# Kernel optimization log

Measured on AMD Instinct MI355X. Metric: run time of the kernel, lower is better.

## Reference

```python
import jax, jax.numpy as jnp
import numpy as np

ROIALIGN = (7, 7)   # args.roialign_size
SCALE = 0.125       # args.spatial_scale
SR = 2              # roi_align sampling ratio (fixed; torchvision uses adaptive when -1)


def _conv2d(x, w, b, pad):
    y = jax.lax.conv_general_dilated(x, w, (1, 1), pad,
                                     dimension_numbers=('NCHW', 'OIHW', 'NCHW'))
    return y + b[None, :, None, None]


def _bilinear(f, ys, xs):
    # f: [C,H,W]; ys: [Ny]; xs: [Nx] -> [C,Ny,Nx]
    C, H, W = f.shape
    y = jnp.clip(ys, 0.0, H - 1.0)
    x = jnp.clip(xs, 0.0, W - 1.0)
    y0 = jnp.floor(y).astype(jnp.int32)
    x0 = jnp.floor(x).astype(jnp.int32)
    y1 = jnp.minimum(y0 + 1, H - 1)
    x1 = jnp.minimum(x0 + 1, W - 1)
    wy = (y - y0)[None, :, None]
    wx = (x - x0)[None, None, :]
    f00 = f[:, y0[:, None], x0[None, :]]
    f01 = f[:, y0[:, None], x1[None, :]]
    f10 = f[:, y1[:, None], x0[None, :]]
    f11 = f[:, y1[:, None], x1[None, :]]
    return f00 * (1 - wy) * (1 - wx) + f01 * (1 - wy) * wx + f10 * wy * (1 - wx) + f11 * wy * wx


def _roi_align(feat, rois):
    # feat: [N,C,H,W]; rois: [K,5] = (batch_idx, x1, y1, x2, y2) in image coords
    rh, rw = ROIALIGN
    C = feat.shape[1]

    def one(box, bidx):
        f = feat[bidx]
        x1, y1, x2, y2 = box * SCALE
        bh = (y2 - y1) / rh
        bw = (x2 - x1) / rw
        ys = y1 + (jnp.arange(rh * SR, dtype=feat.dtype) + 0.5) / SR * bh
        xs = x1 + (jnp.arange(rw * SR, dtype=feat.dtype) + 0.5) / SR * bw
        s = _bilinear(f, ys, xs)                       # [C, rh*SR, rw*SR]
        return s.reshape(C, rh, SR, rw, SR).mean(axis=(2, 4))

    return jax.vmap(one)(rois[:, 1:5], rois[:, 0].astype(jnp.int32))


def setup_inputs() -> dict:
    key = jax.random.key(0)
    ks = jax.random.split(key, 16)
    N, M, H, W = 4, 48, 96, 96
    cor_planes = 4 * (2 * 4 + 1) ** 2  # 324
    corr = jax.random.normal(ks[0], (N, cor_planes, H, W), jnp.float32)

    def make_det(k):
        k1, k2, k3, k4, k5, k6 = jax.random.split(k, 6)
        cx = jax.random.uniform(k1, (N, M), minval=80.0, maxval=688.0)
        cy = jax.random.uniform(k2, (N, M), minval=80.0, maxval=688.0)
        w = jax.random.uniform(k3, (N, M), minval=24.0, maxval=120.0)
        h = jax.random.uniform(k4, (N, M), minval=24.0, maxval=120.0)
        valid = jnp.where(jax.random.uniform(k5, (N, M)) < 0.9, 1.0, -1.0)
        ids = jax.random.randint(k6, (N, M), 0, 100).astype(jnp.float32)
        pad = jnp.zeros((N, M, 4), jnp.float32)
        cols = [valid, ids, cx, cy, w, h]
        return jnp.concatenate([c[..., None] for c in cols] + [pad], axis=-1)

    detection1 = make_det(ks[1])
    detection2 = make_det(ks[2])

    def p(k, shape):
        return (jax.random.normal(k, shape, jnp.float32) * 0.02)

    return {
        'corr': corr,
        'detection1_': detection1,
        'detection1': detection1,
        'detection2': detection2,
        'convc1_w': p(ks[3], (256, cor_planes, 1, 1)), 'convc1_b': jnp.zeros(256, jnp.float32),
        'convc2_w': p(ks[4], (256, 256, 3, 3)), 'convc2_b': jnp.zeros(256, jnp.float32),
        'conv_w': p(ks[5], (128, 256, 3, 3)), 'conv_b': jnp.zeros(128, jnp.float32),
        'head_conv_w': p(ks[6], (256, 132, 7, 7)), 'head_conv_b': jnp.zeros(256, jnp.float32),
        'fc6_w': p(ks[7], (256, 256)), 'fc6_b': jnp.zeros(256, jnp.float32),
        'fc7_w': p(ks[8], (256, 256)), 'fc7_b': jnp.zeros(256, jnp.float32),
        'cls_w': p(ks[9], (1, 256)), 'cls_b': jnp.zeros(1, jnp.float32),
    }


def reference(corr, detection1_, detection1, detection2,
              convc1_w, convc1_b, convc2_w, convc2_b, conv_w, conv_b,
              head_conv_w, head_conv_b, fc6_w, fc6_b, fc7_w, fc7_b, cls_w, cls_b):
    N, M = detection1.shape[0], detection1.shape[1]
    rh, rw = ROIALIGN
    # CompressConv
    c = jax.nn.relu(_conv2d(corr, convc1_w, convc1_b, 'VALID'))
    c = jax.nn.relu(_conv2d(c, convc2_w, convc2_b, [(1, 1), (1, 1)]))
    rel = jax.nn.relu(_conv2d(c, conv_w, conv_b, [(1, 1), (1, 1)]))   # [N,128,H,W]

    def to_xyxy(d):
        xy1 = d[..., 2:4] - d[..., 4:6] / 2
        xy2 = xy1 + d[..., 4:6]
        return jnp.concatenate([d[..., :2], xy1, xy2, d[..., 6:]], axis=-1)

    d1 = to_xyxy(detection1)
    d2 = to_xyxy(detection2)
    bidx = jnp.broadcast_to(jnp.arange(N, dtype=d1.dtype)[:, None], (N, M))
    rois = jnp.concatenate([bidx[..., None], d1[..., 2:6]], axis=-1).reshape(N * M, 5)
    rf = _roi_align(rel, rois)                                        # [N*M,128,7,7]

    d_ = jnp.concatenate([
        jnp.broadcast_to(d1[..., :8][:, :, None, :], (N, M, M, 8)),
        jnp.broadcast_to(d2[..., :8][:, None, :, :], (N, M, M, 8)),
    ], axis=-1).reshape(N * M * M, 16)

    # position encoding: 4 relative-geometry channels tiled over the ROI grid
    eps = 1e-6
    cx1 = (d_[:, 2] + d_[:, 4]) * 0.5; cy1 = (d_[:, 3] + d_[:, 5]) * 0.5
    w1 = jnp.maximum(d_[:, 4] - d_[:, 2], eps); h1 = jnp.maximum(d_[:, 5] - d_[:, 3], eps)
    cx2 = (d_[:, 10] + d_[:, 12]) * 0.5; cy2 = (d_[:, 11] + d_[:, 13]) * 0.5
    w2 = jnp.maximum(d_[:, 12] - d_[:, 10], eps); h2 = jnp.maximum(d_[:, 13] - d_[:, 11], eps)
    pos4 = jnp.stack([(cx2 - cx1) / w1, (cy2 - cy1) / h1,
                      jnp.log(w2 / w1), jnp.log(h2 / h1)], axis=-1)   # [NMM,4]
    pos = jnp.broadcast_to(pos4[:, :, None, None], (N * M * M, 4, rh, rw))

    rf_exp = jnp.broadcast_to(rf[:, None], (N * M, M, 128, rh, rw)).reshape(N * M * M, 128, rh, rw)
    data = jnp.concatenate([rf_exp, pos], axis=1)                     # [NMM,132,7,7]

    labels = (d_[:, 1] == d_[:, 9]).astype(jnp.float32)
    valid = (d_[:, 0] != -1) & (d_[:, 8] != -1)

    # ConvMLPHead (scores for invalid pairs are simply masked out by `valid`)
    x = _conv2d(data, head_conv_w, head_conv_b, 'VALID').reshape(N * M * M, -1)
    x = jax.nn.relu(x @ fc6_w.T + fc6_b)
    x = jax.nn.relu(x @ fc7_w.T + fc7_b)
    scores = x @ cls_w.T + cls_b                                      # [NMM,1]
    return scores, labels, valid
```

## Files before the change

kernel.cpp:

```cpp
#include <hip/hip_runtime.h>
#include <hip/hip_bf16.h>

#define NB    4
#define HH    96
#define WW    96
#define PIX   9216
#define C0    324
#define MM    48
#define NROI  192
#define NPAIR 9216
#define KHEAD 6468
#define KRF   6272
#define SPLITS 28
#define CPS    7

#define CWSTG 18432

typedef unsigned short u16;
typedef __attribute__((ext_vector_type(8))) short bf16x8;
typedef __attribute__((ext_vector_type(4))) float f32x4;
typedef __attribute__((ext_vector_type(16))) float f32x16;
typedef __attribute__((ext_vector_type(4))) unsigned short u16x4;
typedef __attribute__((ext_vector_type(4))) int i32x4;

__device__ __forceinline__ u16 f2bf(float f) {
    __hip_bfloat16 h = __float2bfloat16(f);
    union { __hip_bfloat16 h; u16 u; } c; c.h = h; return c.u;
}
__device__ __forceinline__ float b2f(u16 u) {
    union { unsigned int i; float f; } c; c.i = ((unsigned int)u) << 16; return c.f;
}

__global__ __launch_bounds__(256) void zero_halo(u16* __restrict__ a1, u16* __restrict__ a2)
{
    int idx = blockIdx.x * 256 + threadIdx.x;
    int c8 = idx & 31;
    int t = idx >> 5;
    int h = t % 388, img = t / 388;
    u16* base = (img & 4) ? a2 : a1;
    int b = img & 3;
    int y, x;
    if (h < 98)       { y = 0;  x = h; }
    else if (h < 196) { y = 97; x = h - 98; }
    else { int r = (h - 196) >> 1; x = ((h - 196) & 1) * 97; y = 1 + r; }
    long long off = (((long long)(b * 98 + y)) * 98 + x) * 256 + c8 * 8;
    i32x4 z = {0, 0, 0, 0};
    *(i32x4*)(base + off) = z;
}

__global__ __launch_bounds__(256) void prep_all(
    const float* __restrict__ c1w, const float* __restrict__ c2w,
    const float* __restrict__ c3w, const float* __restrict__ hw,
    const float* __restrict__ f6w, const float* __restrict__ f7w,
    u16* __restrict__ wt1f, u16* __restrict__ wt2f, u16* __restrict__ wt3f,
    u16* __restrict__ wtHt, u16* __restrict__ w6c, u16* __restrict__ w7c,
    float* __restrict__ wsum4)
{
    int blk = blockIdx.x, tid = threadIdx.x;
    if (blk < 352) {
        int idx = blk * 256 + tid;
        if (idx >= 90112) return;
        int j = idx & 7, lane = (idx >> 3) & 63, ot = (idx >> 9) & 7, ks = idx >> 12;
        int oc = ot * 32 + (lane & 31);
        int k = ks * 16 + (lane >> 5) * 8 + j;
        wt1f[idx] = f2bf((k < C0) ? c1w[oc * C0 + k] : 0.f);
    } else if (blk < 2656) {
        int idx = (blk - 352) * 256 + tid;
        int j = idx & 7, lane = (idx >> 3) & 63, ot = (idx >> 9) & 3;
        int t = idx >> 11;
        int tap = t % 9; t /= 9;
        int icb = t & 15, ocb = t >> 4;
        int oc = ocb * 128 + ot * 32 + (lane & 31);
        int ic = icb * 16 + (lane >> 5) * 8 + j;
        wt2f[idx] = f2bf(c2w[(oc * 256 + ic) * 9 + tap]);
    } else if (blk < 3808) {
        int idx = (blk - 2656) * 256 + tid;
        int j = idx & 7, lane = (idx >> 3) & 63, ot = (idx >> 9) & 3;
        int t = idx >> 11;
        int tap = t % 9; int icb = t / 9;
        int oc = ot * 32 + (lane & 31);
        int ic = icb * 16 + (lane >> 5) * 8 + j;
        wt3f[idx] = f2bf(c3w[(oc * 256 + ic) * 9 + tap]);
    } else if (blk < 10080) {
        int idx = (blk - 3808) * 256 + tid;
        int oc = idx / KRF, r = idx % KRF;
        int s = r >> 7, c = r & 127;
        wtHt[idx] = f2bf(hw[oc * KHEAD + c * 49 + s]);
    } else if (blk < 10336) {
        int idx = (blk - 10080) * 256 + tid;
        w6c[idx] = f2bf(f6w[idx]);
    } else if (blk < 10592) {
        int idx = (blk - 10336) * 256 + tid;
        w7c[idx] = f2bf(f7w[idx]);
    } else {
        int idx = (blk - 10592) * 256 + tid;
        if (idx >= 1024) return;
        int oc = idx >> 2, j = idx & 3;
        const float* p = hw + (long long)oc * KHEAD + (128 + j) * 49;
        float s = 0.f;
        #pragma unroll
        for (int t = 0; t < 49; ++t) s += p[t];
        wsum4[idx] = s;
    }
}

__global__ __launch_bounds__(256) void conv1_v2(
    const float* __restrict__ corr, const u16* __restrict__ wf,
    const float* __restrict__ bias, u16* __restrict__ outp)
{
    __shared__ __align__(16) u16 Ws1[8192];
    __shared__ __align__(16) u16 Bs[64 * 40];
    const int tid = threadIdx.x;
    const int b = blockIdx.y;
    const int p0 = blockIdx.x * 64;
    const int lane = tid & 63, wid = tid >> 6;
    const int n = lane & 31, half = lane >> 5;
    const int wocw = wid & 1, wpx = wid >> 1;
    const int kr = tid >> 3, pxg = tid & 7;

    f32x16 acc[4];
    #pragma unroll
    for (int i = 0; i < 4; ++i)
        #pragma unroll
        for (int e = 0; e < 16; ++e) acc[i][e] = 0.f;

    float4 s0 = {0,0,0,0}, s1 = {0,0,0,0};
    if (kr < C0) {
        const float* src = &corr[((long long)(b * C0 + kr)) * PIX + p0 + pxg * 8];
        s0 = *(const float4*)src; s1 = *(const float4*)(src + 4);
    }
    bf16x8 wr[4];
    #pragma unroll
    for (int i = 0; i < 4; ++i) wr[i] = *(const bf16x8*)(wf + (i * 256 + tid) * 8);

    for (int kc = 0; kc < 11; ++kc) {
        __syncthreads();
        Bs[(pxg * 8 + 0) * 40 + kr] = f2bf(s0.x);
        Bs[(pxg * 8 + 1) * 40 + kr] = f2bf(s0.y);
        Bs[(pxg * 8 + 2) * 40 + kr] = f2bf(s0.z);
        Bs[(pxg * 8 + 3) * 40 + kr] = f2bf(s0.w);
        Bs[(pxg * 8 + 4) * 40 + kr] = f2bf(s1.x);
        Bs[(pxg * 8 + 5) * 40 + kr] = f2bf(s1.y);
        Bs[(pxg * 8 + 6) * 40 + kr] = f2bf(s1.z);
        Bs[(pxg * 8 + 7) * 40 + kr] = f2bf(s1.w);
        #pragma unroll
        for (int i = 0; i < 4; ++i) *(bf16x8*)&Ws1[(i * 256 + tid) * 8] = wr[i];
        __syncthreads();
        if (kc < 10) {
            int k = (kc + 1) * 32 + kr;
            if (k < C0) {
                const float* src = &corr[((long long)(b * C0 + k)) * PIX + p0 + pxg * 8];
                s0 = *(const float4*)src; s1 = *(const float4*)(src + 4);
            } else { s0 = (float4){0,0,0,0}; s1 = (float4){0,0,0,0}; }
            const u16* wn = wf + (kc + 1) * 8192;
            #pragma unroll
            for (int i = 0; i < 4; ++i) wr[i] = *(const bf16x8*)(wn + (i * 256 + tid) * 8);
        }
        #pragma unroll
        for (int ks = 0; ks < 2; ++ks) {
            bf16x8 bb = *(const bf16x8*)&Bs[(wpx * 32 + n) * 40 + ks * 16 + half * 8];
            #pragma unroll
            for (int ot = 0; ot < 4; ++ot) {
                bf16x8 a = *(const bf16x8*)&Ws1[((ks * 8 + wocw * 4 + ot) * 64 + lane) * 8];
                acc[ot] = __builtin_amdgcn_mfma_f32_32x32x16_bf16(a, bb, acc[ot], 0, 0, 0);
            }
        }
    }
    const int px = p0 + wpx * 32 + n;
    const int y = px / 96, x = px % 96;
    const long long obase = (((long long)(b * 98 + y + 1)) * 98 + x + 1) * 256;
    #pragma unroll
    for (int ot = 0; ot < 4; ++ot) {
        int ocb = wocw * 128 + ot * 32;
        f32x16 d = acc[ot];
        #pragma unroll
        for (int r2 = 0; r2 < 4; ++r2) {
            int oc4 = ocb + r2 * 8 + half * 4;
            f32x4 bv = *(const f32x4*)(bias + oc4);
            u16x4 pk;
            #pragma unroll
            for (int g = 0; g < 4; ++g) pk[g] = f2bf(fmaxf(d[r2 * 4 + g] + bv[g], 0.f));
            *(u16x4*)(outp + obase + oc4) = pk;
        }
    }
}

template<int COUT, bool PADOUT>
__global__ __launch_bounds__(256, 2) void conv3x3_v2(
    const u16* __restrict__ inp, const u16* __restrict__ wf,
    const float* __restrict__ bias, u16* __restrict__ outp)
{
    __shared__ __align__(16) u16 Ws[CWSTG];
    __shared__ __align__(16) u16 Hs[204 * 24];
    const int tid = threadIdx.x;
    const int b = blockIdx.z;
    const int x0 = (blockIdx.x % 3) * 32, y0 = (blockIdx.x / 3) * 4;
    const int lane = tid & 63, wid = tid >> 6;
    const int n = lane & 31, half = lane >> 5;
    const int woc = wid & 1, wpx = wid >> 1;

    const u16* wsrc = wf + (size_t)blockIdx.y * 16 * CWSTG;
    const bool hstager = tid < 204;
    const int hrow = tid / 34, hcol = tid % 34;
    const u16* hsrc = inp + (((size_t)(b * 98 + y0 + hrow)) * 98 + x0 + hcol) * 256;

    f32x16 acc[2][2];
    #pragma unroll
    for (int i = 0; i < 2; ++i)
        #pragma unroll
        for (int r = 0; r < 2; ++r)
            #pragma unroll
            for (int e = 0; e < 16; ++e) acc[i][r][e] = 0.f;

    bf16x8 wreg[9];
    bf16x8 h0, h1;
    #pragma unroll
    for (int it = 0; it < 9; ++it)
        wreg[it] = *(const bf16x8*)(wsrc + (it * 256 + tid) * 8);
    if (hstager) { h0 = *(const bf16x8*)hsrc; h1 = *(const bf16x8*)(hsrc + 8); }

    for (int icb = 0; icb < 16; ++icb) {
        __syncthreads();
        #pragma unroll
        for (int it = 0; it < 9; ++it)
            *(bf16x8*)&Ws[(it * 256 + tid) * 8] = wreg[it];
        if (hstager) {
            *(bf16x8*)&Hs[tid * 24]     = h0;
            *(bf16x8*)&Hs[tid * 24 + 8] = h1;
        }
        __syncthreads();
        if (icb < 15) {
            const u16* wn = wsrc + (size_t)(icb + 1) * CWSTG;
            #pragma unroll
            for (int it = 0; it < 9; ++it)
                wreg[it] = *(const bf16x8*)(wn + (it * 256 + tid) * 8);
            if (hstager) {
                const u16* hn = hsrc + (icb + 1) * 16;
                h0 = *(const bf16x8*)hn; h1 = *(const bf16x8*)(hn + 8);
            }
        }
        bf16x8 bfr[4][3];
        #pragma unroll
        for (int rr = 0; rr < 4; ++rr)
            #pragma unroll
            for (int dx = 0; dx < 3; ++dx)
                bfr[rr][dx] = *(const bf16x8*)&Hs[((wpx * 2 + rr) * 34 + dx + n) * 24 + half * 8];
        #pragma unroll
        for (int tap = 0; tap < 9; ++tap) {
            const int dy = tap / 3, dx = tap % 3;
            bf16x8 a0 = *(const bf16x8*)&Ws[((tap * 4 + woc * 2 + 0) * 64 + lane) * 8];
            bf16x8 a1 = *(const bf16x8*)&Ws[((tap * 4 + woc * 2 + 1) * 64 + lane) * 8];
            #pragma unroll
            for (int r = 0; r < 2; ++r) {
                acc[0][r] = __builtin_amdgcn_mfma_f32_32x32x16_bf16(a0, bfr[r + dy][dx], acc[0][r], 0, 0, 0);
                acc[1][r] = __builtin_amdgcn_mfma_f32_32x32x16_bf16(a1, bfr[r + dy][dx], acc[1][r], 0, 0, 0);
            }
        }
    }
    #pragma unroll
    for (int ot = 0; ot < 2; ++ot) {
        int ocb = blockIdx.y * 128 + woc * 64 + ot * 32;
        #pragma unroll
        for (int r = 0; r < 2; ++r) {
            int y = y0 + wpx * 2 + r;
            int x = x0 + n;
            f32x16 d = acc[ot][r];
            long long obase;
            if (PADOUT) obase = (((long long)(b * 98 + y + 1)) * 98 + x + 1) * COUT;
            else        obase = (((long long)(b * 96 + y)) * 96 + x) * COUT;
            #pragma unroll
            for (int r2 = 0; r2 < 4; ++r2) {
                int oc4 = ocb + r2 * 8 + half * 4;
                f32x4 bv = *(const f32x4*)(bias + oc4);
                u16x4 pk;
                #pragma unroll
                for (int g = 0; g < 4; ++g) pk[g] = f2bf(fmaxf(d[r2 * 4 + g] + bv[g], 0.f));
                *(u16x4*)(outp + obase + oc4) = pk;
            }
        }
    }
}

__global__ __launch_bounds__(256) void roi_align_cl(
    const u16* __restrict__ rel, const float* __restrict__ det1,
    u16* __restrict__ rf)
{
    const int roi = blockIdx.x, tid = threadIdx.x;
    const int c = tid & 127, sb = tid >> 7;
    const int b = roi / MM, m = roi % MM;
    const float* d = det1 + (long long)(b * MM + m) * 10;
    float cx = d[2], cy = d[3], w = d[4], h = d[5];
    float x1f = cx - w * 0.5f, y1f = cy - h * 0.5f;
    float x1 = x1f * 0.125f, y1 = y1f * 0.125f;
    float x2 = (x1f + w) * 0.125f, y2 = (y1f + h) * 0.125f;
    float bh = (y2 - y1) * (1.f / 7.f), bw = (x2 - x1) * (1.f / 7.f);
    const u16* fb = rel + (long long)b * PIX * 128 + c;
    for (int s = sb; s < 49; s += 2) {
        int i = s / 7, j = s % 7;
        float sum = 0.f;
        #pragma unroll
        for (int di = 0; di < 2; ++di) {
            float y = y1 + ((float)(2 * i + di) + 0.5f) * 0.5f * bh;
            y = fminf(fmaxf(y, 0.f), 95.f);
            int yy0 = (int)floorf(y);
            int yy1 = min(yy0 + 1, 95);
            float wy = y - (float)yy0;
            #pragma unroll
            for (int dj = 0; dj < 2; ++dj) {
                float x = x1 + ((float)(2 * j + dj) + 0.5f) * 0.5f * bw;
                x = fminf(fmaxf(x, 0.f), 95.f);
                int xx0 = (int)floorf(x);
                int xx1 = min(xx0 + 1, 95);
                float wx = x - (float)xx0;
                float f00 = b2f(fb[((long long)yy0 * 96 + xx0) * 128]);
                float f01 = b2f(fb[((long long)yy0 * 96 + xx1) * 128]);
                float f10 = b2f(fb[((long long)yy1 * 96 + xx0) * 128]);
                float f11 = b2f(fb[((long long)yy1 * 96 + xx1) * 128]);
                sum += f00 * (1.f - wy) * (1.f - wx) + f01 * (1.f - wy) * wx
                     + f10 * wy * (1.f - wx) + f11 * wy * wx;
            }
        }
        rf[(long long)roi * KRF + s * 128 + c] = f2bf(sum * 0.25f);
    }
}

__global__ __launch_bounds__(256) void head_gemm_mfma(
    const u16* __restrict__ rf, const u16* __restrict__ wtHt,
    float* __restrict__ Gpart)
{
    __shared__ __align__(16) u16 As[64 * 40];
    __shared__ __align__(16) u16 Bs[128 * 40];
    const int tid = threadIdx.x;
    const int rb = blockIdx.x >> 1, ob = blockIdx.x & 1;
    const int split = blockIdx.y;
    const int lane = tid & 63, wid = tid >> 6;
    const int q = lane >> 4, m16 = lane & 15;
    const int wr = wid & 1, wo = wid >> 1;

    const int arl = tid >> 2, aqd = tid & 3;
    const u16* abase = rf + (long long)(rb * 64 + arl) * KRF + aqd * 8;
    const int bol0 = tid >> 2, bqd = tid & 3;
    const u16* bbase0 = wtHt + (long long)(ob * 128 + bol0) * KRF + bqd * 8;
    const u16* bbase1 = bbase0 + 64LL * KRF;

    f32x4 acc[2][4];
    #pragma unroll
    for (int i = 0; i < 2; ++i)
        #pragma unroll
        for (int j = 0; j < 4; ++j) acc[i][j] = (f32x4){0.f, 0.f, 0.f, 0.f};

    int k0 = split * CPS * 32;
    bf16x8 ra = *(const bf16x8*)(abase + k0);
    bf16x8 rb0 = *(const bf16x8*)(bbase0 + k0);
    bf16x8 rb1 = *(const bf16x8*)(bbase1 + k0);
    for (int cch = 0; cch < CPS; ++cch) {
        __syncthreads();
        *(bf16x8*)&As[arl * 40 + aqd * 8] = ra;
        *(bf16x8*)&Bs[bol0 * 40 + bqd * 8] = rb0;
        *(bf16x8*)&Bs[(64 + bol0) * 40 + bqd * 8] = rb1;
        __syncthreads();
        if (cch < CPS - 1) {
            int kn = k0 + (cch + 1) * 32;
            ra  = *(const bf16x8*)(abase + kn);
            rb0 = *(const bf16x8*)(bbase0 + kn);
            rb1 = *(const bf16x8*)(bbase1 + kn);
        }
        bf16x8 a[2], bb[4];
        #pragma unroll
        for (int rt = 0; rt < 2; ++rt)
            a[rt] = *(const bf16x8*)&As[(wr * 32 + rt * 16 + m16) * 40 + q * 8];
        #pragma unroll
        for (int ot = 0; ot < 4; ++ot)
            bb[ot] = *(const bf16x8*)&Bs[(wo * 64 + ot * 16 + m16) * 40 + q * 8];
        #pragma unroll
        for (int rt = 0; rt < 2; ++rt)
            #pragma unroll
            for (int ot = 0; ot < 4; ++ot)
                acc[rt][ot] = __builtin_amdgcn_mfma_f32_16x16x32_bf16(a[rt], bb[ot], acc[rt][ot], 0, 0, 0);
    }
    #pragma unroll
    for (int rt = 0; rt < 2; ++rt)
        #pragma unroll
        for (int ot = 0; ot < 4; ++ot) {
            int oc = ob * 128 + wo * 64 + ot * 16 + m16;
            #pragma unroll
            for (int rg = 0; rg < 4; ++rg) {
                int roi = rb * 64 + wr * 32 + rt * 16 + q * 4 + rg;
                Gpart[((long long)split * NROI + roi) * 256 + oc] = acc[rt][ot][rg];
            }
        }
}

__global__ __launch_bounds__(256) void reduce_G_kernel(
    const float* __restrict__ Gpart, float* __restrict__ G)
{
    int idx = blockIdx.x * 256 + threadIdx.x;
    float s = 0.f;
    #pragma unroll
    for (int sp = 0; sp < SPLITS; ++sp) s += Gpart[(long long)sp * NROI * 256 + idx];
    G[idx] = s;
}

#define PHS 272
__global__ __launch_bounds__(256) void pair_head(
    const float* __restrict__ G, const float* __restrict__ d1,
    const float* __restrict__ d2, const float* __restrict__ wsum4,
    const float* __restrict__ hb,
    const u16* __restrict__ w6, const float* __restrict__ b6,
    const u16* __restrict__ w7, const float* __restrict__ b7,
    const float* __restrict__ cw, const float* __restrict__ cb,
    float* __restrict__ scores, float* __restrict__ labels,
    float* __restrict__ valid)
{
    __shared__ __align__(16) u16 bufA[64 * PHS];
    __shared__ __align__(16) u16 bufB[64 * PHS];
    __shared__ float Gs[2][256];
    __shared__ float ps[64][4];
    __shared__ float clw[256];

    const int tid = threadIdx.x;
    const int p0 = blockIdx.x * 64;
    const int r0 = p0 / MM;
    const int lane = tid & 63, w = tid >> 6;
    const int q = lane >> 4, m16 = lane & 15;

    clw[tid] = cw[tid];
    #pragma unroll
    for (int l = 0; l < 2; ++l) {
        int idx = tid + l * 256;
        int rr = idx >> 8, col = idx & 255;
        Gs[rr][col] = G[min(r0 + rr, NROI - 1) * 256 + col];
    }
    if (tid < 64) {
        int pair = p0 + tid;
        int b = pair / (MM * MM); int rem = pair % (MM * MM);
        int m1 = rem / MM, m2 = rem % MM;
        const float* rA = d1 + (long long)(b * MM + m1) * 10;
        const float* rB = d2 + (long long)(b * MM + m2) * 10;
        float v1 = rA[0], id1 = rA[1], cxa = rA[2], cya = rA[3], wa = rA[4], ha = rA[5];
        float v2 = rB[0], id2 = rB[1], cxb = rB[2], cyb = rB[3], wb = rB[4], hbv = rB[5];
        const float eps = 1e-6f;
        float ax1 = cxa - wa * 0.5f, ay1 = cya - ha * 0.5f;
        float ax2 = ax1 + wa,        ay2 = ay1 + ha;
        float bx1 = cxb - wb * 0.5f, by1 = cyb - hbv * 0.5f;
        float bx2 = bx1 + wb,        by2 = by1 + hbv;
        float ccx1 = (ax1 + ax2) * 0.5f, ccy1 = (ay1 + ay2) * 0.5f;
        float ww1 = fmaxf(ax2 - ax1, eps), hh1 = fmaxf(ay2 - ay1, eps);
        float ccx2 = (bx1 + bx2) * 0.5f, ccy2 = (by1 + by2) * 0.5f;
        float ww2 = fmaxf(bx2 - bx1, eps), hh2 = fmaxf(by2 - by1, eps);
        ps[tid][0] = (ccx2 - ccx1) / ww1;
        ps[tid][1] = (ccy2 - ccy1) / hh1;
        ps[tid][2] = logf(ww2 / ww1);
        ps[tid][3] = logf(hh2 / hh1);
        labels[pair] = (id1 == id2) ? 1.f : 0.f;
        valid[pair]  = (v1 != -1.f && v2 != -1.f) ? 1.f : 0.f;
    }
    __syncthreads();

    #pragma unroll
    for (int it = 0; it < 16; ++it) {
        int idx = tid + it * 256;
        int px = idx >> 6, o4 = (idx & 63) * 4;
        int rl = (p0 + px) / MM - r0;
        f32x4 g = *(const f32x4*)&Gs[rl][o4];
        f32x4 hv = *(const f32x4*)&hb[o4];
        f32x4 p4 = *(const f32x4*)&ps[px][0];
        u16x4 pk;
        #pragma unroll
        for (int j = 0; j < 4; ++j) {
            f32x4 w4 = *(const f32x4*)&wsum4[(o4 + j) * 4];
            float v = g[j] + hv[j] + p4[0] * w4[0] + p4[1] * w4[1] + p4[2] * w4[2] + p4[3] * w4[3];
            pk[j] = f2bf(v);
        }
        *(u16x4*)&bufA[px * PHS + o4] = pk;
    }
    __syncthreads();

    #pragma unroll
    for (int layer = 0; layer < 2; ++layer) {
        const u16* wgt = layer ? w7 : w6;
        const float* bs = layer ? b7 : b6;
        const u16* src = layer ? bufB : bufA;
        u16* dst = layer ? bufA : bufB;
        f32x4 acc[4][4];
        #pragma unroll
        for (int i = 0; i < 4; ++i)
            #pragma unroll
            for (int j = 0; j < 4; ++j) acc[i][j] = (f32x4){0.f, 0.f, 0.f, 0.f};
        #pragma unroll
        for (int kc = 0; kc < 8; ++kc) {
            bf16x8 a[4], bb[4];
            #pragma unroll
            for (int i = 0; i < 4; ++i)
                a[i] = *(const bf16x8*)&wgt[(w * 64 + i * 16 + m16) * 256 + kc * 32 + q * 8];
            #pragma unroll
            for (int pt = 0; pt < 4; ++pt)
                bb[pt] = *(const bf16x8*)&src[(pt * 16 + m16) * PHS + kc * 32 + q * 8];
            #pragma unroll
            for (int i = 0; i < 4; ++i)
                #pragma unroll
                for (int pt = 0; pt < 4; ++pt)
                    acc[i][pt] = __builtin_amdgcn_mfma_f32_16x16x32_bf16(a[i], bb[pt], acc[i][pt], 0, 0, 0);
        }
        #pragma unroll
        for (int i = 0; i < 4; ++i) {
            int oc4 = w * 64 + i * 16 + q * 4;
            f32x4 bv = *(const f32x4*)(bs + oc4);
            #pragma unroll
            for (int pt = 0; pt < 4; ++pt) {
                int px = pt * 16 + m16;
                f32x4 dd = acc[i][pt];
                u16x4 pk;
                #pragma unroll
                for (int rg = 0; rg < 4; ++rg)
                    pk[rg] = f2bf(fmaxf(dd[rg] + bv[rg], 0.f));
                *(u16x4*)&dst[px * PHS + oc4] = pk;
            }
        }
        __syncthreads();
    }

    {
        int px = tid >> 2, qq = tid & 3;
        float acc = 0.f;
        #pragma unroll
        for (int k8 = 0; k8 < 8; ++k8) {
            bf16x8 hv = *(const bf16x8*)&bufA[px * PHS + qq * 64 + k8 * 8];
            #pragma unroll
            for (int e = 0; e < 8; ++e)
                acc += b2f((u16)hv[e]) * clw[qq * 64 + k8 * 8 + e];
        }
        acc += __shfl_xor(acc, 1, 64);
        acc += __shfl_xor(acc, 2, 64);
        if (qq == 0) scores[p0 + px] = acc + cb[0];
    }
}

extern "C" void kernel_launch(void* const* d_in, const int* in_sizes, int n_in,
                              void* d_out, int out_size, void* d_ws, size_t ws_size,
                              hipStream_t stream) {
    const float* corr   = (const float*)d_in[0];
    const float* det1   = (const float*)d_in[2];
    const float* det2   = (const float*)d_in[3];
    const float* c1w    = (const float*)d_in[4];
    const float* c1b    = (const float*)d_in[5];
    const float* c2w    = (const float*)d_in[6];
    const float* c2b    = (const float*)d_in[7];
    const float* c3w    = (const float*)d_in[8];
    const float* c3b    = (const float*)d_in[9];
    const float* hw     = (const float*)d_in[10];
    const float* hbias  = (const float*)d_in[11];
    const float* f6w    = (const float*)d_in[12];
    const float* f6b    = (const float*)d_in[13];
    const float* f7w    = (const float*)d_in[14];
    const float* f7b    = (const float*)d_in[15];
    const float* clsw   = (const float*)d_in[16];
    const float* clsb   = (const float*)d_in[17];
    float* out = (float*)d_out;

    char* base = (char*)d_ws;
    auto alloc = [&](size_t bytes) { char* p = base; base += (bytes + 255) & ~(size_t)255; return p; };

    const size_t ACTP_BYTES = (size_t)NB * 98 * 98 * 256 * 2;
    u16*   act1p = (u16*)  alloc(ACTP_BYTES);
    u16*   act2p = (u16*)  alloc(ACTP_BYTES);
    u16*   rel   = (u16*)  alloc((size_t)NB * PIX * 128 * 2);
    u16*   wt1f  = (u16*)  alloc((size_t)90112 * 2);
    u16*   wt2f  = (u16*)  alloc((size_t)2 * 16 * CWSTG * 2);
    u16*   wt3f  = (u16*)  alloc((size_t)16 * CWSTG * 2);
    u16*   wtHt  = (u16*)  alloc((size_t)256 * KRF * 2);
    u16*   w6c   = (u16*)  alloc(256 * 256 * 2);
    u16*   w7c   = (u16*)  alloc(256 * 256 * 2);
    float* wsum4 = (float*)alloc(256 * 4 * 4);
    u16*   rf    = (u16*)  alloc((size_t)NROI * KRF * 2);
    float* Gpart = (float*)alloc((size_t)SPLITS * NROI * 256 * 4);
    float* G     = (float*)alloc(NROI * 256 * 4);

    float* scores_out = out;
    float* labels_out = out + NPAIR;
    float* valid_out  = out + 2 * NPAIR;

    zero_halo<<<388, 256, 0, stream>>>(act1p, act2p);
    prep_all<<<10596, 256, 0, stream>>>(c1w, c2w, c3w, hw, f6w, f7w,
                                        wt1f, wt2f, wt3f, wtHt, w6c, w7c, wsum4);
    conv1_v2<<<dim3(144, NB), 256, 0, stream>>>(corr, wt1f, c1b, act1p);
    conv3x3_v2<256, true><<<dim3(72, 2, NB), 256, 0, stream>>>(act1p, wt2f, c2b, act2p);
    conv3x3_v2<128, false><<<dim3(72, 1, NB), 256, 0, stream>>>(act2p, wt3f, c3b, rel);
    roi_align_cl<<<NROI, 256, 0, stream>>>(rel, det1, rf);
    head_gemm_mfma<<<dim3(6, SPLITS), 256, 0, stream>>>(rf, wtHt, Gpart);
    reduce_G_kernel<<<NROI, 256, 0, stream>>>(Gpart, G);
    pair_head<<<144, 256, 0, stream>>>(G, det1, det2, wsum4, hbias,
                                       w6c, f6b, w7c, f7b, clsw, clsb,
                                       scores_out, labels_out, valid_out);
}
```

Measured before the change: 289.3 us.

## Merge halo zeroing into LDS-staged weight prep, fuse G reduction into pair head

The weight-prep kernel is rewritten so each block loads contiguous float4 rows into shared memory and writes transposed bf16 fragments as 8-wide vectors. This replaces the scattered per-element gathers and cuts the grid from about 10.6k blocks to 732, and it also absorbs the halo-zeroing kernel. The split-K reduction of G is folded into pair_head, which removes a launch and an intermediate buffer, but each pair_head block now reads all 28 partial sums for its ROIs redundantly. The conv3x3 kernel preloads all 18 A fragments from LDS before the MFMA loop, which adds register pressure under launch_bounds(256,2).

```diff
diff --git a/kernel.cpp b/kernel.cpp
--- a/kernel.cpp
+++ b/kernel.cpp
@@ -21,6 +21,7 @@
 typedef __attribute__((ext_vector_type(4))) float f32x4;
 typedef __attribute__((ext_vector_type(16))) float f32x16;
 typedef __attribute__((ext_vector_type(4))) unsigned short u16x4;
+typedef __attribute__((ext_vector_type(8))) unsigned short u16x8;
 typedef __attribute__((ext_vector_type(4))) int i32x4;
 
 __device__ __forceinline__ u16 f2bf(float f) {
@@ -31,76 +32,143 @@
     union { unsigned int i; float f; } c; c.i = ((unsigned int)u) << 16; return c.f;
 }
 
-__global__ __launch_bounds__(256) void zero_halo(u16* __restrict__ a1, u16* __restrict__ a2)
-{
-    int idx = blockIdx.x * 256 + threadIdx.x;
-    int c8 = idx & 31;
-    int t = idx >> 5;
-    int h = t % 388, img = t / 388;
-    u16* base = (img & 4) ? a2 : a1;
-    int b = img & 3;
-    int y, x;
-    if (h < 98)       { y = 0;  x = h; }
-    else if (h < 196) { y = 97; x = h - 98; }
-    else { int r = (h - 196) >> 1; x = ((h - 196) & 1) * 97; y = 1 + r; }
-    long long off = (((long long)(b * 98 + y)) * 98 + x) * 256 + c8 * 8;
-    i32x4 z = {0, 0, 0, 0};
-    *(i32x4*)(base + off) = z;
-}
-
-__global__ __launch_bounds__(256) void prep_all(
+__global__ __launch_bounds__(256) void prep_v2(
     const float* __restrict__ c1w, const float* __restrict__ c2w,
     const float* __restrict__ c3w, const float* __restrict__ hw,
     const float* __restrict__ f6w, const float* __restrict__ f7w,
     u16* __restrict__ wt1f, u16* __restrict__ wt2f, u16* __restrict__ wt3f,
     u16* __restrict__ wtHt, u16* __restrict__ w6c, u16* __restrict__ w7c,
-    float* __restrict__ wsum4)
+    float* __restrict__ wsum4, u16* __restrict__ a1, u16* __restrict__ a2)
 {
-    int blk = blockIdx.x, tid = threadIdx.x;
-    if (blk < 352) {
-        int idx = blk * 256 + tid;
-        if (idx >= 90112) return;
-        int j = idx & 7, lane = (idx >> 3) & 63, ot = (idx >> 9) & 7, ks = idx >> 12;
-        int oc = ot * 32 + (lane & 31);
-        int k = ks * 16 + (lane >> 5) * 8 + j;
-        wt1f[idx] = f2bf((k < C0) ? c1w[oc * C0 + k] : 0.f);
-    } else if (blk < 2656) {
-        int idx = (blk - 352) * 256 + tid;
-        int j = idx & 7, lane = (idx >> 3) & 63, ot = (idx >> 9) & 3;
-        int t = idx >> 11;
-        int tap = t % 9; t /= 9;
-        int icb = t & 15, ocb = t >> 4;
-        int oc = ocb * 128 + ot * 32 + (lane & 31);
-        int ic = icb * 16 + (lane >> 5) * 8 + j;
-        wt2f[idx] = f2bf(c2w[(oc * 256 + ic) * 9 + tap]);
-    } else if (blk < 3808) {
-        int idx = (blk - 2656) * 256 + tid;
-        int j = idx & 7, lane = (idx >> 3) & 63, ot = (idx >> 9) & 3;
-        int t = idx >> 11;
-        int tap = t % 9; int icb = t / 9;
-        int oc = ot * 32 + (lane & 31);
-        int ic = icb * 16 + (lane >> 5) * 8 + j;
-        wt3f[idx] = f2bf(c3w[(oc * 256 + ic) * 9 + tap]);
-    } else if (blk < 10080) {
-        int idx = (blk - 3808) * 256 + tid;
-        int oc = idx / KRF, r = idx % KRF;
-        int s = r >> 7, c = r & 127;
-        wtHt[idx] = f2bf(hw[oc * KHEAD + c * 49 + s]);
-    } else if (blk < 10336) {
-        int idx = (blk - 10080) * 256 + tid;
-        w6c[idx] = f2bf(f6w[idx]);
-    } else if (blk < 10592) {
-        int idx = (blk - 10336) * 256 + tid;
-        w7c[idx] = f2bf(f7w[idx]);
+    __shared__ u16 L[18432];
+    const int blk = blockIdx.x, tid = threadIdx.x;
+
+    if (blk < 8) {
+        const int ot = blk;
+        const float* src = c1w + (size_t)ot * 32 * C0;
+        for (int it = 0; it < 11; ++it) {
+            int i = tid + it * 256;
+            if (i < 2592) {
+                float4 v = *(const float4*)(src + i * 4);
+                int n = i / 81, k4 = (i % 81) * 4;
+                L[n * 324 + k4 + 0] = f2bf(v.x);
+                L[n * 324 + k4 + 1] = f2bf(v.y);
+                L[n * 324 + k4 + 2] = f2bf(v.z);
+                L[n * 324 + k4 + 3] = f2bf(v.w);
+            }
+        }
+        __syncthreads();
+        for (int it = 0; it < 6; ++it) {
+            int v = tid + it * 256;
+            if (v >= 1408) break;
+            int ks = v >> 6, lane = v & 63;
+            int n = lane & 31, half = lane >> 5;
+            u16x8 pk;
+            #pragma unroll
+            for (int j = 0; j < 8; ++j) {
+                int k = ks * 16 + half * 8 + j;
+                pk[j] = (k < C0) ? L[n * 324 + k] : (u16)0;
+            }
+            *(u16x8*)&wt1f[((ks * 8 + ot) * 64 + lane) * 8] = pk;
+        }
+    } else if (blk < 56) {
+        const bool is2 = blk < 40;
+        const int b8 = is2 ? (blk - 8) : (blk - 40);
+        const int oc8 = b8 * 8;
+        const int ocb = oc8 >> 7;
+        const int ot = (oc8 >> 5) & 3;
+        const int nb = oc8 & 31;
+        const float* src = (is2 ? c2w : c3w) + (size_t)oc8 * 2304;
+        u16* dst = is2 ? wt2f : wt3f;
+        for (int it = 0; it < 18; ++it) {
+            int i = tid + it * 256;
+            float4 v = *(const float4*)(src + i * 4);
+            int n = i / 576, t4 = (i % 576) * 4;
+            L[n * 2304 + t4 + 0] = f2bf(v.x);
+            L[n * 2304 + t4 + 1] = f2bf(v.y);
+            L[n * 2304 + t4 + 2] = f2bf(v.z);
+            L[n * 2304 + t4 + 3] = f2bf(v.w);
+        }
+        __syncthreads();
+        for (int it = 0; it < 9; ++it) {
+            int v = tid + it * 256;
+            int o8 = v & 7; int rest = v >> 3;
+            int half = rest & 1; rest >>= 1;
+            int tap = rest % 9; int icb = rest / 9;
+            int lane = half * 32 + nb + o8;
+            u16x8 pk;
+            #pragma unroll
+            for (int j = 0; j < 8; ++j) {
+                int ic = icb * 16 + half * 8 + j;
+                pk[j] = L[o8 * 2304 + ic * 9 + tap];
+            }
+            size_t dest = ((((size_t)(ocb * 16 + icb) * 9 + tap) * 4 + ot) * 64 + lane) * 8;
+            *(u16x8*)&dst[dest] = pk;
+        }
+    } else if (blk < 312) {
+        const int oc = blk - 56;
+        const float* src = hw + (size_t)oc * KHEAD;
+        for (int it = 0; it < 7; ++it) {
+            int i = tid + it * 256;
+            if (i < 1617) {
+                float4 v = *(const float4*)(src + i * 4);
+                L[i * 4 + 0] = f2bf(v.x);
+                L[i * 4 + 1] = f2bf(v.y);
+                L[i * 4 + 2] = f2bf(v.z);
+                L[i * 4 + 3] = f2bf(v.w);
+            }
+        }
+        if (tid < 4) {
+            const float* p = src + (128 + tid) * 49;
+            float s = 0.f;
+            #pragma unroll
+            for (int t = 0; t < 49; ++t) s += p[t];
+            wsum4[oc * 4 + tid] = s;
+        }
+        __syncthreads();
+        for (int it = 0; it < 4; ++it) {
+            int v = tid + it * 256;
+            if (v >= 784) break;
+            u16x8 pk;
+            #pragma unroll
+            for (int j = 0; j < 8; ++j) {
+                int r = v * 8 + j;
+                int s = r >> 7, c = r & 127;
+                pk[j] = L[c * 49 + s];
+            }
+            *(u16x8*)&wtHt[(size_t)oc * KRF + v * 8] = pk;
+        }
+    } else if (blk < 344) {
+        const bool is6 = blk < 328;
+        const int b = is6 ? (blk - 312) : (blk - 328);
+        const float* src = (is6 ? f6w : f7w) + (size_t)(b * 256 + tid) * 16;
+        u16* dst = (is6 ? w6c : w7c) + (size_t)(b * 256 + tid) * 16;
+        u16x8 pk0, pk1;
+        #pragma unroll
+        for (int h = 0; h < 2; ++h) {
+            float4 v0 = *(const float4*)(src + h * 8);
+            float4 v1 = *(const float4*)(src + h * 8 + 4);
+            u16x8 pk;
+            pk[0] = f2bf(v0.x); pk[1] = f2bf(v0.y); pk[2] = f2bf(v0.z); pk[3] = f2bf(v0.w);
+            pk[4] = f2bf(v1.x); pk[5] = f2bf(v1.y); pk[6] = f2bf(v1.z); pk[7] = f2bf(v1.w);
+            if (h == 0) pk0 = pk; else pk1 = pk;
+        }
+        *(u16x8*)(dst + 0) = pk0;
+        *(u16x8*)(dst + 8) = pk1;
     } else {
-        int idx = (blk - 10592) * 256 + tid;
-        if (idx >= 1024) return;
-        int oc = idx >> 2, j = idx & 3;
-        const float* p = hw + (long long)oc * KHEAD + (128 + j) * 49;
-        float s = 0.f;
-        #pragma unroll
-        for (int t = 0; t < 49; ++t) s += p[t];
-        wsum4[idx] = s;
+        int idx = (blk - 344) * 256 + tid;
+        int c8 = idx & 31;
+        int t = idx >> 5;
+        int h = t % 388, img = t / 388;
+        u16* base = (img & 4) ? a2 : a1;
+        int b = img & 3;
+        int y, x;
+        if (h < 98)       { y = 0;  x = h; }
+        else if (h < 196) { y = 97; x = h - 98; }
+        else { int r = (h - 196) >> 1; x = ((h - 196) & 1) * 97; y = 1 + r; }
+        long long off = (((long long)(b * 98 + y)) * 98 + x) * 256 + c8 * 8;
+        i32x4 z = {0, 0, 0, 0};
+        *(i32x4*)(base + off) = z;
     }
 }
 
@@ -186,7 +254,7 @@
 }
 
 template<int COUT, bool PADOUT>
-__global__ __launch_bounds__(256, 2) void conv3x3_v2(
+__global__ __launch_bounds__(256, 2) void conv3x3_v3(
     const u16* __restrict__ inp, const u16* __restrict__ wf,
     const float* __restrict__ bias, u16* __restrict__ outp)
 {
@@ -239,6 +307,12 @@
                 h0 = *(const bf16x8*)hn; h1 = *(const bf16x8*)(hn + 8);
             }
         }
+        bf16x8 afr[9][2];
+        #pragma unroll
+        for (int tap = 0; tap < 9; ++tap)
+            #pragma unroll
+            for (int j = 0; j < 2; ++j)
+                afr[tap][j] = *(const bf16x8*)&Ws[((tap * 4 + woc * 2 + j) * 64 + lane) * 8];
         bf16x8 bfr[4][3];
         #pragma unroll
         for (int rr = 0; rr < 4; ++rr)
@@ -248,12 +322,10 @@
         #pragma unroll
         for (int tap = 0; tap < 9; ++tap) {
             const int dy = tap / 3, dx = tap % 3;
-            bf16x8 a0 = *(const bf16x8*)&Ws[((tap * 4 + woc * 2 + 0) * 64 + lane) * 8];
-            bf16x8 a1 = *(const bf16x8*)&Ws[((tap * 4 + woc * 2 + 1) * 64 + lane) * 8];
             #pragma unroll
             for (int r = 0; r < 2; ++r) {
-                acc[0][r] = __builtin_amdgcn_mfma_f32_32x32x16_bf16(a0, bfr[r + dy][dx], acc[0][r], 0, 0, 0);
-                acc[1][r] = __builtin_amdgcn_mfma_f32_32x32x16_bf16(a1, bfr[r + dy][dx], acc[1][r], 0, 0, 0);
+                acc[0][r] = __builtin_amdgcn_mfma_f32_32x32x16_bf16(afr[tap][0], bfr[r + dy][dx], acc[0][r], 0, 0, 0);
+                acc[1][r] = __builtin_amdgcn_mfma_f32_32x32x16_bf16(afr[tap][1], bfr[r + dy][dx], acc[1][r], 0, 0, 0);
             }
         }
     }
@@ -391,19 +463,9 @@
         }
 }
 
-__global__ __launch_bounds__(256) void reduce_G_kernel(
-    const float* __restrict__ Gpart, float* __restrict__ G)
-{
-    int idx = blockIdx.x * 256 + threadIdx.x;
-    float s = 0.f;
-    #pragma unroll
-    for (int sp = 0; sp < SPLITS; ++sp) s += Gpart[(long long)sp * NROI * 256 + idx];
-    G[idx] = s;
-}
-
 #define PHS 272
 __global__ __launch_bounds__(256) void pair_head(
-    const float* __restrict__ G, const float* __restrict__ d1,
+    const float* __restrict__ Gpart, const float* __restrict__ d1,
     const float* __restrict__ d2, const float* __restrict__ wsum4,
     const float* __restrict__ hb,
     const u16* __restrict__ w6, const float* __restrict__ b6,
@@ -429,7 +491,12 @@
     for (int l = 0; l < 2; ++l) {
         int idx = tid + l * 256;
         int rr = idx >> 8, col = idx & 255;
-        Gs[rr][col] = G[min(r0 + rr, NROI - 1) * 256 + col];
+        int roi = min(r0 + rr, NROI - 1);
+        float s = 0.f;
+        #pragma unroll
+        for (int sp = 0; sp < SPLITS; ++sp)
+            s += Gpart[((long long)sp * NROI + roi) * 256 + col];
+        Gs[rr][col] = s;
     }
     if (tid < 64) {
         int pair = p0 + tid;
@@ -574,22 +641,20 @@
     float* wsum4 = (float*)alloc(256 * 4 * 4);
     u16*   rf    = (u16*)  alloc((size_t)NROI * KRF * 2);
     float* Gpart = (float*)alloc((size_t)SPLITS * NROI * 256 * 4);
-    float* G     = (float*)alloc(NROI * 256 * 4);
 
     float* scores_out = out;
     float* labels_out = out + NPAIR;
     float* valid_out  = out + 2 * NPAIR;
 
-    zero_halo<<<388, 256, 0, stream>>>(act1p, act2p);
-    prep_all<<<10596, 256, 0, stream>>>(c1w, c2w, c3w, hw, f6w, f7w,
-                                        wt1f, wt2f, wt3f, wtHt, w6c, w7c, wsum4);
+    prep_v2<<<732, 256, 0, stream>>>(c1w, c2w, c3w, hw, f6w, f7w,
+                                     wt1f, wt2f, wt3f, wtHt, w6c, w7c, wsum4,
+                                     act1p, act2p);
     conv1_v2<<<dim3(144, NB), 256, 0, stream>>>(corr, wt1f, c1b, act1p);
-    conv3x3_v2<256, true><<<dim3(72, 2, NB), 256, 0, stream>>>(act1p, wt2f, c2b, act2p);
-    conv3x3_v2<128, false><<<dim3(72, 1, NB), 256, 0, stream>>>(act2p, wt3f, c3b, rel);
+    conv3x3_v3<256, true><<<dim3(72, 2, NB), 256, 0, stream>>>(act1p, wt2f, c2b, act2p);
+    conv3x3_v3<128, false><<<dim3(72, 1, NB), 256, 0, stream>>>(act2p, wt3f, c3b, rel);
     roi_align_cl<<<NROI, 256, 0, stream>>>(rel, det1, rf);
     head_gemm_mfma<<<dim3(6, SPLITS), 256, 0, stream>>>(rf, wtHt, Gpart);
-    reduce_G_kernel<<<NROI, 256, 0, stream>>>(Gpart, G);
-    pair_head<<<144, 256, 0, stream>>>(G, det1, det2, wsum4, hbias,
+    pair_head<<<144, 256, 0, stream>>>(Gpart, det1, det2, wsum4, hbias,
                                        w6c, f6b, w7c, f7b, clsw, clsb,
                                        scores_out, labels_out, valid_out);
 }
```

Measured after the change: 282.3 us. 2.4% less time.
